# Performance work log

Measured on AMD Instinct MI355X. Metric: run time of the kernel, lower is better.

The kernel has to match this reference:

```python
import jax, jax.numpy as jnp
import numpy as np

NUM_HEADS = 16
DIM = 1024
HID = DIM // NUM_HEADS
B, S = 2, 2048
NEG_INF = -1e30


def setup_inputs() -> dict:
    key = jax.random.key(0)
    ks = jax.random.split(key, 8)
    def xavier(k, shape, fan_in, fan_out):
        limit = np.sqrt(6.0 / (fan_in + fan_out))
        return jax.random.uniform(k, shape, jnp.float32, -limit, limit)
    return {
        "q": jax.random.normal(ks[0], (B, S, DIM), jnp.float32),
        "k": jax.random.normal(ks[1], (B, S, DIM), jnp.float32),
        "v": jax.random.normal(ks[2], (B, S, DIM), jnp.float32),
        "Wq": xavier(ks[3], (1, NUM_HEADS, DIM, HID), DIM, HID),
        "Wk": xavier(ks[4], (1, NUM_HEADS, DIM, HID), DIM, HID),
        "Wv": xavier(ks[5], (1, NUM_HEADS, DIM, HID), DIM, HID),
        "Wo": xavier(ks[6], (1, DIM, DIM), DIM, DIM),
        "mask": jax.random.randint(ks[7], (B, S), 0, 2, jnp.int32),
    }


def reference(q, k, v, Wq, Wk, Wv, Wo, mask):
    b, s, d = q.shape
    norm = jnp.sqrt(jnp.asarray(HID, q.dtype))
    # per-head projections: [B,S,D] x [H,D,hd] -> [B,H,S,hd]
    qh = jnp.einsum('bsd,hde->bhse', q, Wq[0])
    kh = jnp.einsum('bsd,hde->bhse', k, Wk[0])
    vh = jnp.einsum('bsd,hde->bhse', v, Wv[0])
    scores = jnp.einsum('bhse,bhte->bhst', qh, kh) / norm  # [B,H,S,S]
    m = mask.astype(bool)
    # original fills masked rows AND cols with 0.0 (not -inf)
    pad = m[:, None, :, None] | m[:, None, None, :]
    scores = jnp.where(pad, 0.0, scores)
    causal = jnp.triu(jnp.ones((s, s), bool), 1)
    scores = jnp.where(causal, NEG_INF, scores)
    attn = jax.nn.softmax(scores, axis=-1)
    out = jnp.einsum('bhst,bhte->bhse', attn, vh)  # [B,H,S,hd]
    # faithful to original: raw view (memory reinterpretation), NO head transpose
    out = out.reshape(b, s, NUM_HEADS * HID)
    return out @ Wo[0]
```

## Files before the change

### kernel.cpp

```cpp
#include <hip/hip_runtime.h>
#include <hip/hip_bf16.h>

#define BB 2
#define SS 2048
#define DD 1024
#define HH 16
#define HD 64

typedef __attribute__((ext_vector_type(8))) short bf16x8;
typedef __attribute__((ext_vector_type(4))) float floatx4;

__device__ __forceinline__ short f2bf(float x) {
  __hip_bfloat16 h = __float2bfloat16(x);
  return __builtin_bit_cast(short, h);
}

__device__ __forceinline__ void load_lds16(const void* g, void* l) {
  __builtin_amdgcn_global_load_lds(
      (const __attribute__((address_space(1))) unsigned int*)g,
      (__attribute__((address_space(3))) unsigned int*)l, 16, 0, 0);
}

__device__ __forceinline__ float redsum16(float v) {
  v += __shfl_xor(v, 1, 64);
  v += __shfl_xor(v, 2, 64);
  v += __shfl_xor(v, 4, 64);
  v += __shfl_xor(v, 8, 64);
  return v;
}

__global__ __launch_bounds__(256) void prep(
    const float* __restrict__ q, const float* __restrict__ k,
    const float* __restrict__ v, const float* __restrict__ Wq,
    const float* __restrict__ Wk, const float* __restrict__ Wv,
    const float* __restrict__ Wo, short* __restrict__ qo,
    short* __restrict__ ko, short* __restrict__ vo, short* __restrict__ qT,
    short* __restrict__ kT, short* __restrict__ vT, short* __restrict__ WoT) {
  __shared__ short sT[64 * 72];
  const int blk = blockIdx.x;
  if (blk < 12288) {
    const int which = blk >> 12, x = blk & 4095;
    const float* src = which == 0 ? q : which == 1 ? k : v;
    short* dst       = which == 0 ? qo : which == 1 ? ko : vo;
    size_t i = ((size_t)x * 256 + threadIdx.x) * 4;
    float4 f = *(const float4*)(src + i);
    short4 s;
    s.x = f2bf(f.x); s.y = f2bf(f.y); s.z = f2bf(f.z); s.w = f2bf(f.w);
    *(short4*)(dst + i) = s;
    return;
  }
  const int t = threadIdx.x, r = t >> 2, c0 = (t & 3) * 16;
  const float* src;
  short* dst;
  if (blk < 13056) {
    const int b2 = blk - 12288, which = b2 >> 8, rr = b2 & 255;
    const int dtile = rr & 15, h = rr >> 4, d0 = dtile * 64;
    const float* W = which == 0 ? Wq : which == 1 ? Wk : Wv;
    short* WT      = which == 0 ? qT : which == 1 ? kT : vT;
    src = W + ((size_t)h * DD + d0 + r) * HD + c0;
    dst = WT + ((size_t)h * HD + r) * DD + d0 + c0;
  } else {
    const int b3 = blk - 13056;
    const int k0 = (b3 & 15) * 64, n0 = (b3 >> 4) * 64;
    src = Wo + (size_t)(k0 + r) * DD + n0 + c0;
    dst = WoT + (size_t)(n0 + r) * DD + k0 + c0;
  }
  const float4* s4 = (const float4*)src;
  float4 f0 = s4[0], f1 = s4[1], f2 = s4[2], f3 = s4[3];
  const float ff[16] = {f0.x, f0.y, f0.z, f0.w, f1.x, f1.y, f1.z, f1.w,
                        f2.x, f2.y, f2.z, f2.w, f3.x, f3.y, f3.z, f3.w};
#pragma unroll
  for (int j = 0; j < 16; ++j) sT[r * 72 + c0 + j] = f2bf(ff[j]);
  __syncthreads();
  alignas(16) short tmp[16];
#pragma unroll
  for (int j = 0; j < 16; ++j) tmp[j] = sT[(c0 + j) * 72 + r];
  *(int4*)(dst) = *(const int4*)(tmp);
  *(int4*)(dst + 8) = *(const int4*)(tmp + 8);
}

__global__ __launch_bounds__(256) void proj(
    const short* __restrict__ xq, const short* __restrict__ xk,
    const short* __restrict__ xv, const short* __restrict__ WqT,
    const short* __restrict__ WkT, const short* __restrict__ WvT,
    short* __restrict__ qh, short* __restrict__ kh, short* __restrict__ vh) {
  __shared__ short sA[128 * 32];
  __shared__ short sB[128 * 32];
  const int xcd = blockIdx.x & 7, tt = blockIdx.x >> 3;
  const int which = tt >> 5;
  const int rest = tt & 31;
  const int j = ((xcd & 3) << 1) | (rest >> 4);
  const int i = ((xcd >> 2) << 4) | (rest & 15);
  const short* X  = which == 0 ? xq : which == 1 ? xk : xv;
  const short* WT = which == 0 ? WqT : which == 1 ? WkT : WvT;
  short* dst      = which == 0 ? qh : which == 1 ? kh : vh;
  const int m0 = i * 128, n0 = j * 128;
  const int tid = threadIdx.x, wid = tid >> 6, lane = tid & 63;
  const int quad = lane >> 4, l16 = lane & 15;
  const int wr = wid >> 1, wc = wid & 1;

  floatx4 acc[4][4] = {};
  for (int k0 = 0; k0 < DD; k0 += 32) {
    __syncthreads();
#pragma unroll
    for (int ii = 0; ii < 2; ++ii) {
      const int c = wid * 2 + ii;
      const int ci = c * 64 + lane;
      load_lds16(X + (size_t)(m0 + (ci >> 2)) * DD + k0 + (ci & 3) * 8,
                 &sA[c * 512]);
      load_lds16(WT + (size_t)(n0 + (ci >> 2)) * DD + k0 + (ci & 3) * 8,
                 &sB[c * 512]);
    }
    __syncthreads();
    bf16x8 af[4], bfr[4];
#pragma unroll
    for (int mi = 0; mi < 4; ++mi)
      af[mi] = *(const bf16x8*)&sA[(wr * 64 + mi * 16 + l16) * 32 + quad * 8];
#pragma unroll
    for (int ni = 0; ni < 4; ++ni)
      bfr[ni] = *(const bf16x8*)&sB[(wc * 64 + ni * 16 + l16) * 32 + quad * 8];
#pragma unroll
    for (int mi = 0; mi < 4; ++mi)
#pragma unroll
      for (int ni = 0; ni < 4; ++ni)
        acc[mi][ni] = __builtin_amdgcn_mfma_f32_16x16x32_bf16(
            af[mi], bfr[ni], acc[mi][ni], 0, 0, 0);
  }
  const float scale = (which == 0) ? 0.125f : 1.0f;
#pragma unroll
  for (int mi = 0; mi < 4; ++mi)
#pragma unroll
    for (int ni = 0; ni < 4; ++ni)
#pragma unroll
      for (int r2 = 0; r2 < 4; ++r2) {
        const int m = m0 + wr * 64 + mi * 16 + quad * 4 + r2;
        const int n = n0 + wc * 64 + ni * 16 + l16;
        dst[(size_t)m * DD + n] = f2bf(acc[mi][ni][r2] * scale);
      }
}

__global__ __launch_bounds__(256) void vtrans(const short* __restrict__ vh,
                                              short* __restrict__ vhT) {
  __shared__ short sT[64 * 72];
  const int xcd = blockIdx.x & 7, slot = blockIdx.x >> 3;
  const int bh = (xcd << 2) | (slot & 3), stile = slot >> 2;
  const int b = bh >> 4, h = bh & 15, s0 = stile * 64;
  const int t = threadIdx.x, r = t >> 2, c0 = (t & 3) * 16;
  const short* src = vh + (size_t)(b * SS + s0 + r) * DD + h * HD + c0;
  *(int4*)&sT[r * 72 + c0] = *(const int4*)src;
  *(int4*)&sT[r * 72 + c0 + 8] = *(const int4*)(src + 8);
  __syncthreads();
  alignas(16) short tmp[16];
#pragma unroll
  for (int j = 0; j < 16; ++j) tmp[j] = sT[(c0 + j) * 72 + r];
  short* dst = vhT + ((size_t)bh * HD + r) * SS + s0 + c0;
  *(int4*)(dst) = *(const int4*)(tmp);
  *(int4*)(dst + 8) = *(const int4*)(tmp + 8);
}

__global__ __launch_bounds__(256) void attn(
    const short* __restrict__ qh, const short* __restrict__ kh,
    const short* __restrict__ vhT, const int* __restrict__ mask,
    short* __restrict__ X) {
  __shared__ union {
    short sP[4][32 * 72];
    float red[2][40 * 64];
  } u;
  const int tid = threadIdx.x, wid = tid >> 6, lane = tid & 63;
  const int quad = lane >> 4, l16 = lane & 15;
  const int xcd = blockIdx.x & 7, slot = blockIdx.x >> 3;
  const int bh = (xcd << 2) | (slot & 3);
  const int strip = 63 - (slot >> 2);
  const int b = bh >> 4, h = bh & 15;
  const int row0 = strip * 32;

  const short* Q  = qh + (size_t)b * SS * DD + h * HD;
  const short* K  = kh + (size_t)b * SS * DD + h * HD;
  const short* Vt = vhT + (size_t)bh * HD * SS;
  const int* mk = mask + b * SS;

  bf16x8 aq[2][2];
#pragma unroll
  for (int mi = 0; mi < 2; ++mi)
#pragma unroll
    for (int ks = 0; ks < 2; ++ks)
      aq[mi][ks] = *(const bf16x8*)(Q + (size_t)(row0 + mi * 16 + l16) * DD +
                                    ks * 32 + quad * 8);
  int mrow[2][4];
#pragma unroll
  for (int mi = 0; mi < 2; ++mi)
#pragma unroll
    for (int r2 = 0; r2 < 4; ++r2)
      mrow[mi][r2] = mk[row0 + mi * 16 + quad * 4 + r2];

  floatx4 o[2][4] = {};
  float lacc[2][4];
#pragma unroll
  for (int mi = 0; mi < 2; ++mi)
#pragma unroll
    for (int r2 = 0; r2 < 4; ++r2) lacc[mi][r2] = 0.f;

  const int ntiles = (row0 >> 6) + 1;
  for (int tb = wid; tb < ntiles; tb += 4) {
    const int t0 = tb * 64;
    bf16x8 bk[4][2], bv[4][2];
#pragma unroll
    for (int ni = 0; ni < 4; ++ni)
#pragma unroll
      for (int ks = 0; ks < 2; ++ks)
        bk[ni][ks] = *(const bf16x8*)(K + (size_t)(t0 + ni * 16 + l16) * DD +
                                      ks * 32 + quad * 8);
#pragma unroll
    for (int ei = 0; ei < 4; ++ei)
#pragma unroll
      for (int ks = 0; ks < 2; ++ks)
        bv[ei][ks] = *(const bf16x8*)(Vt + (size_t)(ei * 16 + l16) * SS + t0 +
                                      ks * 32 + quad * 8);
    int mt[4];
#pragma unroll
    for (int ni = 0; ni < 4; ++ni) mt[ni] = mk[t0 + ni * 16 + l16];
    const bool diag = (tb == ntiles - 1);

#pragma unroll
    for (int mi = 0; mi < 2; ++mi) {
      floatx4 s[4] = {};
#pragma unroll
      for (int ks = 0; ks < 2; ++ks)
#pragma unroll
        for (int ni = 0; ni < 4; ++ni)
          s[ni] = __builtin_amdgcn_mfma_f32_16x16x32_bf16(
              aq[mi][ks], bk[ni][ks], s[ni], 0, 0, 0);
#pragma unroll
      for (int ni = 0; ni < 4; ++ni)
#pragma unroll
        for (int r2 = 0; r2 < 4; ++r2) {
          float x = s[ni][r2];
          if (mrow[mi][r2] | mt[ni]) x = 0.f;
          float p = __expf(x);
          if (diag) {
            const int row = row0 + mi * 16 + quad * 4 + r2;
            const int col = t0 + ni * 16 + l16;
            if (col > row) p = 0.f;
          }
          lacc[mi][r2] += p;
          u.sP[wid][(mi * 16 + quad * 4 + r2) * 72 + ni * 16 + l16] = f2bf(p);
        }
    }
#pragma unroll
    for (int ks = 0; ks < 2; ++ks) {
      bf16x8 ap[2];
#pragma unroll
      for (int mi = 0; mi < 2; ++mi)
        ap[mi] = *(const bf16x8*)&u.sP[wid][(mi * 16 + l16) * 72 + ks * 32 +
                                            quad * 8];
#pragma unroll
      for (int mi = 0; mi < 2; ++mi)
#pragma unroll
        for (int ei = 0; ei < 4; ++ei)
          o[mi][ei] = __builtin_amdgcn_mfma_f32_16x16x32_bf16(
              ap[mi], bv[ei][ks], o[mi][ei], 0, 0, 0);
    }
  }

  __syncthreads();
  auto dump = [&](float* dst) {
    int j = 0;
#pragma unroll
    for (int mi = 0; mi < 2; ++mi)
#pragma unroll
      for (int ei = 0; ei < 4; ++ei)
#pragma unroll
        for (int r2 = 0; r2 < 4; ++r2) dst[(j++) * 64 + lane] = o[mi][ei][r2];
#pragma unroll
    for (int mi = 0; mi < 2; ++mi)
#pragma unroll
      for (int r2 = 0; r2 < 4; ++r2) dst[(j++) * 64 + lane] = lacc[mi][r2];
  };
  auto accum = [&](const float* srcp) {
    int j = 0;
#pragma unroll
    for (int mi = 0; mi < 2; ++mi)
#pragma unroll
      for (int ei = 0; ei < 4; ++ei)
#pragma unroll
        for (int r2 = 0; r2 < 4; ++r2) o[mi][ei][r2] += srcp[(j++) * 64 + lane];
#pragma unroll
    for (int mi = 0; mi < 2; ++mi)
#pragma unroll
      for (int r2 = 0; r2 < 4; ++r2) lacc[mi][r2] += srcp[(j++) * 64 + lane];
  };
  if (wid == 1) dump(u.red[0]);
  if (wid == 3) dump(u.red[1]);
  __syncthreads();
  if (wid == 0) accum(u.red[0]);
  if (wid == 2) accum(u.red[1]);
  __syncthreads();
  if (wid == 2) dump(u.red[0]);
  __syncthreads();
  if (wid == 0) {
    accum(u.red[0]);
#pragma unroll
    for (int mi = 0; mi < 2; ++mi)
#pragma unroll
      for (int r2 = 0; r2 < 4; ++r2) {
        const float inv = 1.0f / redsum16(lacc[mi][r2]);
        const int srow = row0 + mi * 16 + quad * 4 + r2;
#pragma unroll
        for (int ei = 0; ei < 4; ++ei)
          X[((size_t)bh * SS + srow) * HD + ei * 16 + l16] =
              f2bf(o[mi][ei][r2] * inv);
      }
  }
}

__global__ __launch_bounds__(256) void oproj(const short* __restrict__ X,
                                             const short* __restrict__ WoT,
                                             float* __restrict__ out) {
  __shared__ short sA[128 * 32];
  __shared__ short sB[64 * 32];
  const int m0 = blockIdx.x * 128, n0 = blockIdx.y * 64;
  const int tid = threadIdx.x, wid = tid >> 6, lane = tid & 63;
  const int quad = lane >> 4, l16 = lane & 15;
  const int wr = wid >> 1, wc = wid & 1;

  floatx4 acc[4][2] = {};
  for (int k0 = 0; k0 < DD; k0 += 32) {
    __syncthreads();
#pragma unroll
    for (int i = 0; i < 2; ++i) {
      const int c = wid * 2 + i;
      const int ci = c * 64 + lane;
      load_lds16(X + (size_t)(m0 + (ci >> 2)) * DD + k0 + (ci & 3) * 8,
                 &sA[c * 512]);
    }
    {
      const int ci = wid * 64 + lane;
      load_lds16(WoT + (size_t)(n0 + (ci >> 2)) * DD + k0 + (ci & 3) * 8,
                 &sB[wid * 512]);
    }
    __syncthreads();
    bf16x8 af[4], bfr[2];
#pragma unroll
    for (int mi = 0; mi < 4; ++mi)
      af[mi] = *(const bf16x8*)&sA[(wr * 64 + mi * 16 + l16) * 32 + quad * 8];
#pragma unroll
    for (int ni = 0; ni < 2; ++ni)
      bfr[ni] = *(const bf16x8*)&sB[(wc * 32 + ni * 16 + l16) * 32 + quad * 8];
#pragma unroll
    for (int mi = 0; mi < 4; ++mi)
#pragma unroll
      for (int ni = 0; ni < 2; ++ni)
        acc[mi][ni] = __builtin_amdgcn_mfma_f32_16x16x32_bf16(
            af[mi], bfr[ni], acc[mi][ni], 0, 0, 0);
  }
#pragma unroll
  for (int mi = 0; mi < 4; ++mi)
#pragma unroll
    for (int ni = 0; ni < 2; ++ni)
#pragma unroll
      for (int r2 = 0; r2 < 4; ++r2)
        out[(size_t)(m0 + wr * 64 + mi * 16 + quad * 4 + r2) * DD + n0 +
            wc * 32 + ni * 16 + l16] = acc[mi][ni][r2];
}

extern "C" void kernel_launch(void* const* d_in, const int* in_sizes, int n_in,
                              void* d_out, int out_size, void* d_ws,
                              size_t ws_size, hipStream_t stream) {
  const float* q  = (const float*)d_in[0];
  const float* k  = (const float*)d_in[1];
  const float* v  = (const float*)d_in[2];
  const float* Wq = (const float*)d_in[3];
  const float* Wk = (const float*)d_in[4];
  const float* Wv = (const float*)d_in[5];
  const float* Wo = (const float*)d_in[6];
  const int* mask = (const int*)d_in[7];
  float* out = (float*)d_out;

  short* ws = (short*)d_ws;
  const size_t NIN = (size_t)BB * SS * DD;
  const size_t NWH = (size_t)HH * HD * DD;
  short* qb  = ws;
  short* kb  = ws + NIN;
  short* vb  = ws + 2 * NIN;
  short* WqT = ws + 3 * NIN;
  short* WkT = WqT + NWH;
  short* WvT = WkT + NWH;
  short* WoT = WvT + NWH;
  short* qhp = WoT + (size_t)DD * DD;
  short* khp = qhp + NIN;
  short* vhp = khp + NIN;
  short* Xp  = qb;
  short* vhT = kb;

  prep<<<dim3(13312), 256, 0, stream>>>(q, k, v, Wq, Wk, Wv, Wo, qb, kb, vb,
                                        WqT, WkT, WvT, WoT);
  proj<<<dim3(768), 256, 0, stream>>>(qb, kb, vb, WqT, WkT, WvT, qhp, khp,
                                      vhp);
  vtrans<<<dim3(1024), 256, 0, stream>>>(vhp, vhT);
  attn<<<dim3(2048), 256, 0, stream>>>(qhp, khp, vhT, mask, Xp);
  oproj<<<dim3(32, 16), 256, 0, stream>>>(Xp, WoT, out);
}
```

Measured before the change: 243.4 us.

## Fuse V transpose into projection epilogue and streamline attention masking

The projection kernel now writes the V head output already transposed, staging each block's tile through a padded shared-memory buffer. This removes the separate vtrans kernel launch and the extra global write and read of V. The attention inner loop computes exp unconditionally and selects 1.0 for padded positions, and uses a hand-written round-to-nearest bf16 conversion, to shorten the softmax path. The change adds about 34 KB of shared memory to proj, which may lower occupancy, and the custom conversion does not treat NaN specially.

Result: no change. 242.0 us (-0.6%).

```diff
diff --git a/kernel.cpp b/kernel.cpp
--- a/kernel.cpp
+++ b/kernel.cpp
@@ -13,6 +13,11 @@
 __device__ __forceinline__ short f2bf(float x) {
   __hip_bfloat16 h = __float2bfloat16(x);
   return __builtin_bit_cast(short, h);
+}
+
+__device__ __forceinline__ short f2bf_fast(float x) {
+  unsigned u = __float_as_uint(x);
+  return (short)((u + 0x7FFFu + ((u >> 16) & 1u)) >> 16);
 }
 
 __device__ __forceinline__ void load_lds16(const void* g, void* l) {
@@ -83,9 +88,10 @@
     const short* __restrict__ xq, const short* __restrict__ xk,
     const short* __restrict__ xv, const short* __restrict__ WqT,
     const short* __restrict__ WkT, const short* __restrict__ WvT,
-    short* __restrict__ qh, short* __restrict__ kh, short* __restrict__ vh) {
+    short* __restrict__ qh, short* __restrict__ kh, short* __restrict__ vhT) {
   __shared__ short sA[128 * 32];
   __shared__ short sB[128 * 32];
+  __shared__ short sT2[128 * 136];
   const int xcd = blockIdx.x & 7, tt = blockIdx.x >> 3;
   const int which = tt >> 5;
   const int rest = tt & 31;
@@ -93,7 +99,6 @@
   const int i = ((xcd >> 2) << 4) | (rest & 15);
   const short* X  = which == 0 ? xq : which == 1 ? xk : xv;
   const short* WT = which == 0 ? WqT : which == 1 ? WkT : WvT;
-  short* dst      = which == 0 ? qh : which == 1 ? kh : vh;
   const int m0 = i * 128, n0 = j * 128;
   const int tid = threadIdx.x, wid = tid >> 6, lane = tid & 63;
   const int quad = lane >> 4, l16 = lane & 15;
@@ -126,36 +131,42 @@
         acc[mi][ni] = __builtin_amdgcn_mfma_f32_16x16x32_bf16(
             af[mi], bfr[ni], acc[mi][ni], 0, 0, 0);
   }
-  const float scale = (which == 0) ? 0.125f : 1.0f;
-#pragma unroll
-  for (int mi = 0; mi < 4; ++mi)
-#pragma unroll
-    for (int ni = 0; ni < 4; ++ni)
-#pragma unroll
-      for (int r2 = 0; r2 < 4; ++r2) {
-        const int m = m0 + wr * 64 + mi * 16 + quad * 4 + r2;
-        const int n = n0 + wc * 64 + ni * 16 + l16;
-        dst[(size_t)m * DD + n] = f2bf(acc[mi][ni][r2] * scale);
-      }
-}
-
-__global__ __launch_bounds__(256) void vtrans(const short* __restrict__ vh,
-                                              short* __restrict__ vhT) {
-  __shared__ short sT[64 * 72];
-  const int xcd = blockIdx.x & 7, slot = blockIdx.x >> 3;
-  const int bh = (xcd << 2) | (slot & 3), stile = slot >> 2;
-  const int b = bh >> 4, h = bh & 15, s0 = stile * 64;
-  const int t = threadIdx.x, r = t >> 2, c0 = (t & 3) * 16;
-  const short* src = vh + (size_t)(b * SS + s0 + r) * DD + h * HD + c0;
-  *(int4*)&sT[r * 72 + c0] = *(const int4*)src;
-  *(int4*)&sT[r * 72 + c0 + 8] = *(const int4*)(src + 8);
-  __syncthreads();
-  alignas(16) short tmp[16];
-#pragma unroll
-  for (int j = 0; j < 16; ++j) tmp[j] = sT[(c0 + j) * 72 + r];
-  short* dst = vhT + ((size_t)bh * HD + r) * SS + s0 + c0;
-  *(int4*)(dst) = *(const int4*)(tmp);
-  *(int4*)(dst + 8) = *(const int4*)(tmp + 8);
+  if (which != 2) {
+    short* dst = which == 0 ? qh : kh;
+    const float scale = (which == 0) ? 0.125f : 1.0f;
+#pragma unroll
+    for (int mi = 0; mi < 4; ++mi)
+#pragma unroll
+      for (int ni = 0; ni < 4; ++ni)
+#pragma unroll
+        for (int r2 = 0; r2 < 4; ++r2) {
+          const int m = m0 + wr * 64 + mi * 16 + quad * 4 + r2;
+          const int n = n0 + wc * 64 + ni * 16 + l16;
+          dst[(size_t)m * DD + n] = f2bf(acc[mi][ni][r2] * scale);
+        }
+  } else {
+    __syncthreads();
+#pragma unroll
+    for (int mi = 0; mi < 4; ++mi)
+#pragma unroll
+      for (int ni = 0; ni < 4; ++ni)
+#pragma unroll
+        for (int r2 = 0; r2 < 4; ++r2) {
+          const int ml = wr * 64 + mi * 16 + quad * 4 + r2;
+          const int nl = wc * 64 + ni * 16 + l16;
+          sT2[nl * 136 + ml] = f2bf(acc[mi][ni][r2]);
+        }
+    __syncthreads();
+    const int b = m0 >> 11;
+    const int row = tid >> 1, half = tid & 1;
+    const int h = (n0 + row) >> 6, e = (n0 + row) & 63;
+    short* dstp = vhT + ((size_t)(b * HH + h) * HD + e) * SS + (m0 & 2047) +
+                  half * 64;
+    const short* srcl = &sT2[row * 136 + half * 64];
+#pragma unroll
+    for (int jj = 0; jj < 8; ++jj)
+      *(int4*)(dstp + jj * 8) = *(const int4*)(srcl + jj * 8);
+  }
 }
 
 __global__ __launch_bounds__(256) void attn(
@@ -186,12 +197,12 @@
     for (int ks = 0; ks < 2; ++ks)
       aq[mi][ks] = *(const bf16x8*)(Q + (size_t)(row0 + mi * 16 + l16) * DD +
                                     ks * 32 + quad * 8);
-  int mrow[2][4];
+  bool mrowb[2][4];
 #pragma unroll
   for (int mi = 0; mi < 2; ++mi)
 #pragma unroll
     for (int r2 = 0; r2 < 4; ++r2)
-      mrow[mi][r2] = mk[row0 + mi * 16 + quad * 4 + r2];
+      mrowb[mi][r2] = mk[row0 + mi * 16 + quad * 4 + r2] != 0;
 
   floatx4 o[2][4] = {};
   float lacc[2][4];
@@ -216,9 +227,9 @@
       for (int ks = 0; ks < 2; ++ks)
         bv[ei][ks] = *(const bf16x8*)(Vt + (size_t)(ei * 16 + l16) * SS + t0 +
                                       ks * 32 + quad * 8);
-    int mt[4];
-#pragma unroll
-    for (int ni = 0; ni < 4; ++ni) mt[ni] = mk[t0 + ni * 16 + l16];
+    bool mtb[4];
+#pragma unroll
+    for (int ni = 0; ni < 4; ++ni) mtb[ni] = mk[t0 + ni * 16 + l16] != 0;
     const bool diag = (tb == ntiles - 1);
 
 #pragma unroll
@@ -234,16 +245,17 @@
       for (int ni = 0; ni < 4; ++ni)
 #pragma unroll
         for (int r2 = 0; r2 < 4; ++r2) {
-          float x = s[ni][r2];
-          if (mrow[mi][r2] | mt[ni]) x = 0.f;
-          float p = __expf(x);
+          const float ev = __expf(s[ni][r2]);
+          float p = mtb[ni] ? 1.f : ev;
+          p = mrowb[mi][r2] ? 1.f : p;
           if (diag) {
             const int row = row0 + mi * 16 + quad * 4 + r2;
             const int col = t0 + ni * 16 + l16;
             if (col > row) p = 0.f;
           }
           lacc[mi][r2] += p;
-          u.sP[wid][(mi * 16 + quad * 4 + r2) * 72 + ni * 16 + l16] = f2bf(p);
+          u.sP[wid][(mi * 16 + quad * 4 + r2) * 72 + ni * 16 + l16] =
+              f2bf_fast(p);
         }
     }
 #pragma unroll
@@ -388,15 +400,13 @@
   short* WoT = WvT + NWH;
   short* qhp = WoT + (size_t)DD * DD;
   short* khp = qhp + NIN;
-  short* vhp = khp + NIN;
+  short* vhT = khp + NIN;
   short* Xp  = qb;
-  short* vhT = kb;
 
   prep<<<dim3(13312), 256, 0, stream>>>(q, k, v, Wq, Wk, Wv, Wo, qb, kb, vb,
                                         WqT, WkT, WvT, WoT);
   proj<<<dim3(768), 256, 0, stream>>>(qb, kb, vb, WqT, WkT, WvT, qhp, khp,
-                                      vhp);
-  vtrans<<<dim3(1024), 256, 0, stream>>>(vhp, vhT);
+                                      vhT);
   attn<<<dim3(2048), 256, 0, stream>>>(qhp, khp, vhT, mask, Xp);
   oproj<<<dim3(32, 16), 256, 0, stream>>>(Xp, WoT, out);
 }
```
